# Kernel optimization log

Measured on AMD Instinct MI355X. Metric: run time of the kernel, lower is better.

Reference implementation:

```python
import math
import jax, jax.numpy as jnp
from jax import lax
import numpy as np

TWO_PI = 2.0 * math.pi
CG_ITERS = 30      # DifferentiableLinearSolver(max_iter=30)
CG_TOL = 1e-6
CG_REG = 1e-6      # reg = 1e-6 * I added inside the solver


def build_second_diff_matrix(N, dtype):
    e = jnp.ones(N, dtype)
    e2 = -2.0 * e
    e2 = e2.at[0].set(-1.0).at[-1].set(-1.0)
    oper = jnp.diag(e2) + jnp.diag(e[:-1], -1) + jnp.diag(e[:-1], 1)
    return oper.T @ oper


def cumtrapz(y, dx):
    # cumulative trapezoid along last axis, keeping length (leading zero)
    avg = (y[..., :-1] + y[..., 1:]) * (0.5 * dx)
    c = jnp.cumsum(avg, axis=-1)
    return jnp.concatenate([jnp.zeros_like(y[..., :1]), c], axis=-1)


def differ5(y, delta):
    mid = (y[..., 2:] - y[..., :-2]) / (2.0 * delta)
    first = (y[..., 1:2] - y[..., 0:1]) / delta
    last = (y[..., -1:] - y[..., -2:-1]) / delta
    return jnp.concatenate([first, mid, last], axis=-1)


def projec5(vec, var):
    # per-row norm-ball projection; vec: (B, N)
    M = vec.shape[-1]
    e = jnp.sqrt(M * var)
    n = jnp.linalg.norm(vec, axis=-1, keepdims=True)
    scale = jnp.where(n > e, e / jnp.maximum(n, 1e-30), 1.0)
    return vec * scale


def cg_solve(opedoub, coef, diagv, rhs, x0):
    # Solves (coef*opedoub + diag(diagv) + CG_REG*I) x = rhs via CG,
    # matching torch semantics (early break freezes state).
    def mv(p):
        return coef * (opedoub @ p) + (diagv + CG_REG) * p

    r0 = rhs - mv(x0)
    rs0 = jnp.dot(r0, r0)

    def step(carry, _):
        x, r, p, rsold, done = carry
        Ap = mv(p)
        a = rsold / (jnp.dot(p, Ap) + 1e-12)
        x1 = jnp.where(done, x, x + a * p)
        r1 = jnp.where(done, r, r - a * Ap)
        rsnew = jnp.dot(r1, r1)
        done1 = done | (jnp.sqrt(rsnew) < CG_TOL)
        bta = rsnew / (rsold + 1e-12)
        p1 = jnp.where(done1, p, r1 + bta * p)
        rsold1 = jnp.where(done1, rsold, rsnew)
        return (x1, r1, p1, rsold1, done1), None

    (x, _, _, _, _), _ = lax.scan(step, (x0, r0, r0, rs0, jnp.array(False)), None, length=CG_ITERS)
    return x


def _forward(s, eIF, xm, ym, sum_x, sum_y, lamuda, init_freqs, mode_mask,
             alpha, beta, var, fs, iteration,
             fe_w1, fe_b1, fe_w2, fe_b2,
             pr_w1, pr_b1, pr_w2, pr_b2, pr_w3, pr_b3, iter_weight):
    dtype = s.dtype
    B, N = s.shape
    K = eIF.shape[1]

    # ---- hyperparameter refinement MLP ----
    avg = jnp.mean(init_freqs, axis=1, keepdims=True)              # (B,1)
    h = jax.nn.relu(avg @ fe_w1.T + fe_b1)
    h = jax.nn.relu(h @ fe_w2.T + fe_b2)                            # (B,16)
    cur = jnp.stack([jnp.broadcast_to(alpha, (B,)),
                     jnp.broadcast_to(beta, (B,))], axis=1)         # (B,2)
    z = jnp.concatenate([h, cur], axis=1)                           # (B,18)
    z = jax.nn.relu(z @ pr_w1.T + pr_b1)
    z = jax.nn.relu(z @ pr_w2.T + pr_b2)
    res = jnp.tanh(z @ pr_w3.T + pr_b3)                             # (B,2)
    fac = jax.nn.sigmoid(iter_weight * iteration)
    res = res * fac * 0.1
    new_alpha = jnp.clip(alpha + jnp.mean(res[:, 0] * alpha), 1e-6, 0.01)
    new_beta = jnp.clip(beta + jnp.mean(res[:, 1] * beta), 1e-6, 0.1)

    betathr = jnp.minimum(10.0 ** (iteration / 36.0 - 10.0), new_beta)
    opedoub = build_second_diff_matrix(N, dtype)
    dx = 1.0 / fs

    # Within the torch k-loop, temp sums / lamuda / new_eIF[b,k] all still hold
    # their *input* values, so all (b,k) sub-problems are independent -> vmap.
    u = projec5(s - sum_x - sum_y - lamuda / new_alpha, var)        # (B,N)

    phase = TWO_PI * cumtrapz(eIF, dx)                               # (B,K,N)
    cosm = jnp.cos(phase)
    sinm = jnp.sin(phase)
    resid = (s[:, None, :] - (sum_x[:, None, :] - xm * cosm)
             - (sum_y[:, None, :] - ym * sinm)
             - u[:, None, :] - (lamuda / new_alpha)[:, None, :])
    rhs_x = cosm * resid
    rhs_y = sinm * resid

    coefA = 2.0 / new_alpha
    flat = lambda t: t.reshape(B * K, N)
    cg_v = jax.vmap(cg_solve, in_axes=(None, None, 0, 0, 0))

    xs = cg_v(opedoub, coefA, flat(cosm ** 2), flat(rhs_x), flat(xm)).reshape(B, K, N)
    ys = cg_v(opedoub, coefA, flat(sinm ** 2), flat(rhs_y), flat(ym)).reshape(B, K, N)

    xbar = differ5(xs, dx)
    ybar = differ5(ys, dx)
    denom = xs ** 2 + ys ** 2 + 1e-12
    deltaIF = (xs * ybar - ys * xbar) / (denom * TWO_PI)

    coefS = 2.0 / betathr
    ones_d = jnp.ones((B * K, N), dtype)
    zeros_d = jnp.zeros((B * K, N), dtype)
    smooth = cg_v(opedoub, coefS, ones_d, flat(deltaIF), zeros_d).reshape(B, K, N)
    eIF_s = eIF - 0.5 * smooth

    active = (mode_mask != 0)[:, :, None]                            # (B,K,1)
    new_xm = jnp.where(active, xs, xm)
    new_ym = jnp.where(active, ys, ym)
    new_eIF = jnp.where(active, eIF_s, eIF)

    new_phase = TWO_PI * cumtrapz(new_eIF, dx)
    maskf = active.astype(dtype)
    bsx = jnp.sum(maskf * new_xm * jnp.cos(new_phase), axis=1)       # (B,N)
    bsy = jnp.sum(maskf * new_ym * jnp.sin(new_phase), axis=1)
    new_lamuda = lamuda + new_alpha * (u + bsx + bsy - s)

    return (new_eIF, new_xm, new_ym, bsx, bsy, new_lamuda, new_alpha, new_beta)


def setup_inputs() -> dict:
    key = jax.random.key(0)
    B, K, N = 8, 4, 2048
    ks = jax.random.split(key, 20)
    f32 = jnp.float32
    inp = {
        "s": jax.random.normal(ks[0], (B, N), f32),
        "eIF": 50.0 + 200.0 * jax.random.uniform(ks[1], (B, K, N), f32),
        "xm": 0.1 * jax.random.normal(ks[2], (B, K, N), f32),
        "ym": 0.1 * jax.random.normal(ks[3], (B, K, N), f32),
        "sum_x": 0.1 * jax.random.normal(ks[4], (B, N), f32),
        "sum_y": 0.1 * jax.random.normal(ks[5], (B, N), f32),
        "lamuda": 0.01 * jax.random.normal(ks[6], (B, N), f32),
        "init_freqs": 50.0 + 200.0 * jax.random.uniform(ks[7], (B, K), f32),
        "mode_mask": jnp.ones((B, K), jnp.int32),
        "alpha": jnp.asarray(0.005, f32),
        "beta": jnp.asarray(0.05, f32),
        "var": jnp.asarray(0.01, f32),
        "fs": jnp.asarray(2000.0, f32),
        "iteration": 1,
        # HyperparameterRefinement params (torch Linear: y = x @ W.T + b)
        "fe_w1": 0.1 * jax.random.normal(ks[8], (32, 1), f32),
        "fe_b1": jnp.zeros((32,), f32),
        "fe_w2": 0.1 * jax.random.normal(ks[9], (16, 32), f32),
        "fe_b2": jnp.zeros((16,), f32),
        "pr_w1": 0.1 * jax.random.normal(ks[10], (64, 18), f32),
        "pr_b1": jnp.zeros((64,), f32),
        "pr_w2": 0.1 * jax.random.normal(ks[11], (32, 64), f32),
        "pr_b2": jnp.zeros((32,), f32),
        "pr_w3": 0.1 * jax.random.normal(ks[12], (2, 32), f32),
        "pr_b3": jnp.zeros((2,), f32),
        "iter_weight": jnp.asarray(0.1, f32),
    }
    return inp


def reference(s, eIF, xm, ym, sum_x, sum_y, lamuda, init_freqs, mode_mask,
              alpha, beta, var, fs, iteration,
              fe_w1, fe_b1, fe_w2, fe_b2,
              pr_w1, pr_b1, pr_w2, pr_b2, pr_w3, pr_b3, iter_weight):
    return _forward(s, eIF, xm, ym, sum_x, sum_y, lamuda, init_freqs, mode_mask,
                    alpha, beta, var, fs, iteration,
                    fe_w1, fe_b1, fe_w2, fe_b2,
                    pr_w1, pr_b1, pr_w2, pr_b2, pr_w3, pr_b3, iter_weight)
```

## Files before the change

### kernel.cpp

```cpp
#include <hip/hip_runtime.h>
#include <math.h>

#define Nq 2048
#define Bq 8
#define Kq 4
#define BKq 32
#define NE 16
#define TWO_PI_D 6.283185307179586
#define PI_D 3.141592653589793
#define INV2PI_D 0.15915494309189535


__device__ __forceinline__ double wave_sum_d(double v) {
#pragma unroll
  for (int off = 1; off < 64; off <<= 1) v += __shfl_xor(v, off, 64);
  return v;
}

__device__ __forceinline__ float dpp_sum_f32(float v) {
  v += __int_as_float(__builtin_amdgcn_update_dpp(0, __float_as_int(v), 0x111, 0xf, 0xf, false));
  v += __int_as_float(__builtin_amdgcn_update_dpp(0, __float_as_int(v), 0x112, 0xf, 0xf, false));
  v += __int_as_float(__builtin_amdgcn_update_dpp(0, __float_as_int(v), 0x114, 0xf, 0xe, false));
  v += __int_as_float(__builtin_amdgcn_update_dpp(0, __float_as_int(v), 0x118, 0xf, 0xc, false));
  v += __int_as_float(__builtin_amdgcn_update_dpp(0, __float_as_int(v), 0x142, 0xa, 0xf, false));
  v += __int_as_float(__builtin_amdgcn_update_dpp(0, __float_as_int(v), 0x143, 0xc, 0xf, false));
  return __int_as_float(__builtin_amdgcn_readlane(__float_as_int(v), 63));
}

__device__ __forceinline__ float dpp_up1(float v) {
  return __int_as_float(__builtin_amdgcn_update_dpp(0, __float_as_int(v), 0x138, 0xf, 0xf, false));
}
__device__ __forceinline__ float dpp_dn1(float v) {
  return __int_as_float(__builtin_amdgcn_update_dpp(0, __float_as_int(v), 0x130, 0xf, 0xf, false));
}

__device__ __forceinline__ double lane_excl_prefix_d(double T, int lane) {
  double acc = T;
#pragma unroll
  for (int off = 1; off < 64; off <<= 1) {
    double t = __shfl_up(acc, off, 64);
    if (lane >= off) acc += t;
  }
  return acc - T;
}

__device__ __forceinline__ void fast_sincos_ph(double ph, float* sn, float* cs) {
  double k = trunc(ph * INV2PI_D);
  float phr = (float)(ph - k * TWO_PI_D);
  __sincosf(phr, sn, cs);
}

template <bool UNIT>
__device__ __forceinline__ void applyA16(const float* p, float* Ap,
                                         const float* dd, float c, float c3,
                                         float c4, float ddu, float hL0,
                                         float hL1, float hR0, float hR1,
                                         int lane, int half) {
  float lm1 = dpp_up1(p[NE - 1]);
  float lm2 = dpp_up1(p[NE - 2]);
  float rp1 = dpp_dn1(p[0]);
  float rp2 = dpp_dn1(p[1]);
  if (lane == 0) { lm1 = hL1; lm2 = hL0; }
  if (lane == 63) { rp1 = hR0; rp2 = hR1; }
#pragma unroll
  for (int e = 0; e < NE; ++e) {
    float m2 = (e >= 2) ? p[e - 2] : (e == 1 ? lm1 : lm2);
    float m1 = (e >= 1) ? p[e - 1] : lm1;
    float q1 = (e <= NE - 2) ? p[e + 1] : rp1;
    float q2 = (e <= NE - 3) ? p[e + 2] : (e == NE - 2 ? rp1 : rp2);
    float u = fmaf(c, m2 + q2, -(c4 * (m1 + q1)));
    Ap[e] = fmaf(UNIT ? ddu : dd[e], p[e], u);
  }
  if (half == 0 && lane == 0) {
    float d0 = (UNIT ? ddu : dd[0]) - c4;
    Ap[0] = fmaf(d0, p[0], fmaf(c, p[2], -(c3 * p[1])));
    float d1 = UNIT ? ddu : dd[1];
    Ap[1] = fmaf(d1, p[1], -(c3 * p[0])) + fmaf(c, p[3], -(c4 * p[2]));
  }
  if (half == 1 && lane == 63) {
    float dm2 = UNIT ? ddu : dd[NE - 2];
    Ap[NE - 2] = fmaf(dm2, p[NE - 2], c * p[NE - 4]) -
                 fmaf(c4, p[NE - 3], c3 * p[NE - 1]);
    float dm1 = (UNIT ? ddu : dd[NE - 1]) - c4;
    Ap[NE - 1] = fmaf(dm1, p[NE - 1], c * p[NE - 3]) - c3 * p[NE - 2];
  }
}

template <bool UNIT>
__device__ __forceinline__ void cg_wave2(float coef, float* dd, float* r,
                                         float* x, float hxL0, float hxL1,
                                         float hxR0, float hxR1, int lane,
                                         int half, int wv,
                                         float (*sh_part)[4],
                                         float (*sh_rb)[2]) {
  const float c = coef, c3 = 3.0f * coef, c4 = 4.0f * coef;
  const float ddu = 6.0f * coef + (1.0f + 1e-6f);
  if (!UNIT) {
#pragma unroll
    for (int e = 0; e < NE; ++e) dd[e] += 6.0f * coef;
  }
  const int nb = wv ^ 1;
  float p[NE], Ap[NE];
  applyA16<UNIT>(x, Ap, dd, c, c3, c4, ddu, hxL0, hxL1, hxR0, hxR1, lane, half);
  float s0 = 0.f, s1 = 0.f;
#pragma unroll
  for (int e = 0; e < NE; ++e) {
    r[e] -= Ap[e];
    p[e] = r[e];
    ((e & 1) ? s1 : s0) = fmaf(r[e], r[e], (e & 1) ? s1 : s0);
  }
  float rsp = dpp_sum_f32(s0 + s1);
  if (lane == 0) sh_part[wv][3] = rsp;
  if (half == 0) {
    if (lane == 63) { sh_rb[wv][0] = r[NE - 2]; sh_rb[wv][1] = r[NE - 1]; }
  } else {
    if (lane == 0) { sh_rb[wv][0] = r[0]; sh_rb[wv][1] = r[1]; }
  }
  __syncthreads();
  float rs = rsp + sh_part[nb][3];
  float hL0 = 0.f, hL1 = 0.f, hR0 = 0.f, hR1 = 0.f;
  if (half == 1) { hL0 = sh_rb[nb][0]; hL1 = sh_rb[nb][1]; }
  else { hR0 = sh_rb[nb][0]; hR1 = sh_rb[nb][1]; }
  bool done = false;
  for (int it = 0; it < 30; ++it) {
    applyA16<UNIT>(p, Ap, dd, c, c3, c4, ddu, hL0, hL1, hR0, hR1, lane, half);
    float pa0 = 0.f, pa1 = 0.f, aa0 = 0.f, aa1 = 0.f, ra0 = 0.f, ra1 = 0.f;
#pragma unroll
    for (int e = 0; e < NE; ++e) {
      if (e & 1) {
        pa1 = fmaf(p[e], Ap[e], pa1);
        aa1 = fmaf(Ap[e], Ap[e], aa1);
        ra1 = fmaf(r[e], Ap[e], ra1);
      } else {
        pa0 = fmaf(p[e], Ap[e], pa0);
        aa0 = fmaf(Ap[e], Ap[e], aa0);
        ra0 = fmaf(r[e], Ap[e], ra0);
      }
    }
    float papp = dpp_sum_f32(pa0 + pa1);
    float aapp = dpp_sum_f32(aa0 + aa1);
    float rapp = dpp_sum_f32(ra0 + ra1);
    if (lane == 0) {
      sh_part[wv][0] = papp;
      sh_part[wv][1] = aapp;
      sh_part[wv][2] = rapp;
    }
    __syncthreads();
    float pap = papp + sh_part[nb][0];
    float apap = aapp + sh_part[nb][1];
    float rap = rapp + sh_part[nb][2];
    float a = __fdividef(rs, pap + 1e-12f);
    float rsnew = fmaf(a * a, apap, fmaf(-2.0f * a, rap, rs));
    if (!done) {
#pragma unroll
      for (int e = 0; e < NE; ++e) {
        x[e] = fmaf(a, p[e], x[e]);
        r[e] = fmaf(-a, Ap[e], r[e]);
      }
    }
    bool done1 = done || (rsnew < 1e-12f);
    float bta = __fdividef(rsnew, rs + 1e-12f);
    if (!done1) {
#pragma unroll
      for (int e = 0; e < NE; ++e) p[e] = fmaf(bta, p[e], r[e]);
      rs = rsnew;
      if (half == 0) {
        if (lane == 63) { sh_rb[wv][0] = r[NE - 2]; sh_rb[wv][1] = r[NE - 1]; }
      } else {
        if (lane == 0) { sh_rb[wv][0] = r[0]; sh_rb[wv][1] = r[1]; }
      }
    }
    __syncthreads();
    if (!done1) {
      if (half == 1) {
        hL0 = fmaf(bta, hL0, sh_rb[nb][0]);
        hL1 = fmaf(bta, hL1, sh_rb[nb][1]);
      } else {
        hR0 = fmaf(bta, hR0, sh_rb[nb][0]);
        hR1 = fmaf(bta, hR1, sh_rb[nb][1]);
      }
    }
    done = done1;
  }
}

__device__ __forceinline__ double blk_reduce(double v, double* sh) {
#pragma unroll
  for (int off = 32; off > 0; off >>= 1) v += __shfl_down(v, off, 64);
  int wid = threadIdx.x >> 6;
  int lane = threadIdx.x & 63;
  __syncthreads();
  if (lane == 0) sh[wid] = v;
  __syncthreads();
  double r = sh[0] + sh[1] + sh[2] + sh[3];
  __syncthreads();
  return r;
}

__global__ __launch_bounds__(256, 1) void row_kernel(
    const float* __restrict__ s, const float* __restrict__ eIF,
    const float* __restrict__ xm, const float* __restrict__ ym,
    const float* __restrict__ sum_x, const float* __restrict__ sum_y,
    const float* __restrict__ lamuda, const float* __restrict__ init_freqs,
    const int* __restrict__ mode_mask, const float* __restrict__ alpha_p,
    const float* __restrict__ beta_p, const float* __restrict__ var_p,
    const float* __restrict__ fs_p, const int* __restrict__ iter_p,
    const float* __restrict__ fe_w1, const float* __restrict__ fe_b1,
    const float* __restrict__ fe_w2, const float* __restrict__ fe_b2,
    const float* __restrict__ pr_w1, const float* __restrict__ pr_b1,
    const float* __restrict__ pr_w2, const float* __restrict__ pr_b2,
    const float* __restrict__ pr_w3, const float* __restrict__ pr_b3,
    const float* __restrict__ iter_w_p, double* __restrict__ hdr,
    float* __restrict__ out_eIF, float* __restrict__ out_xm,
    float* __restrict__ out_ym, float* __restrict__ cx_w,
    float* __restrict__ cy_w, float* __restrict__ out_scal) {
  __shared__ double sh_avg[Bq];
  __shared__ double sh_h1[Bq][32];
  __shared__ double sh_z[Bq][18];
  __shared__ double sh_z1[Bq][64];
  __shared__ double sh_z2[Bq][32];
  __shared__ double sh_res[Bq][2];
  __shared__ double sh_hdr[4];
  __shared__ double sh_sc[8];
  __shared__ float sh_part[4][4];
  __shared__ float sh_rb[4][2];
  __shared__ float sh_xs[Nq], sh_ys[Nq];

  const int tid = threadIdx.x;
  const int wv = tid >> 6, lane = tid & 63;
  const int pair = wv >> 1, half = wv & 1;
  const int row = blockIdx.x, b = row >> 2;
  const int bb = b * Nq, base = row * Nq;
  const int seg0 = half * 1024;

  double alpha = (double)alpha_p[0], beta = (double)beta_p[0];
  double iterv = (double)iter_p[0];
  if (tid < Bq) {
    double avg = 0.0;
#pragma unroll
    for (int k = 0; k < Kq; ++k) avg += (double)init_freqs[tid * Kq + k];
    sh_avg[tid] = avg * (1.0 / Kq);
  }
  __syncthreads();
  {
    int b2 = tid >> 5, j = tid & 31;
    double v = (double)fe_w1[j] * sh_avg[b2] + (double)fe_b1[j];
    sh_h1[b2][j] = v > 0.0 ? v : 0.0;
  }
  __syncthreads();
  if (tid < 128) {
    int b2 = tid >> 4, j = tid & 15;
    double acc = (double)fe_b2[j];
    for (int i = 0; i < 32; ++i) acc += (double)fe_w2[j * 32 + i] * sh_h1[b2][i];
    sh_z[b2][j] = acc > 0.0 ? acc : 0.0;
  }
  if (tid >= 128 && tid < 128 + Bq) {
    sh_z[tid - 128][16] = alpha;
    sh_z[tid - 128][17] = beta;
  }
  __syncthreads();
  for (int n = tid; n < 512; n += 256) {
    int b2 = n >> 6, j = n & 63;
    double acc = (double)pr_b1[j];
    for (int i = 0; i < 18; ++i) acc += (double)pr_w1[j * 18 + i] * sh_z[b2][i];
    sh_z1[b2][j] = acc > 0.0 ? acc : 0.0;
  }
  __syncthreads();
  {
    int b2 = tid >> 5, j = tid & 31;
    double acc = (double)pr_b2[j];
    for (int i = 0; i < 64; ++i) acc += (double)pr_w2[j * 64 + i] * sh_z1[b2][i];
    sh_z2[b2][j] = acc > 0.0 ? acc : 0.0;
  }
  __syncthreads();
  if (tid < 16) {
    int b2 = tid >> 1, c = tid & 1;
    double acc = (double)pr_b3[c];
    for (int i = 0; i < 32; ++i) acc += (double)pr_w3[c * 32 + i] * sh_z2[b2][i];
    double fac = 1.0 / (1.0 + exp(-(double)iter_w_p[0] * iterv));
    sh_res[b2][c] = tanh(acc) * fac * 0.1;
  }
  __syncthreads();
  if (tid == 0) {
    double r0 = 0.0, r1 = 0.0;
    for (int q = 0; q < Bq; ++q) { r0 += sh_res[q][0]; r1 += sh_res[q][1]; }
    double na = fmin(fmax(alpha + r0 * alpha * (1.0 / Bq), 1e-6), 0.01);
    double nb2 = fmin(fmax(beta + r1 * beta * (1.0 / Bq), 1e-6), 0.1);
    double betathr = fmin(pow(10.0, iterv / 36.0 - 10.0), nb2);
    sh_hdr[0] = na;
    sh_hdr[1] = 2.0 / na;
    sh_hdr[2] = 2.0 / betathr;
    sh_hdr[3] = 1.0 / na;
    hdr[0] = na;
    hdr[4] = 1.0 / na;
    out_scal[0] = (float)na;
    out_scal[1] = (float)nb2;
  }
  __syncthreads();
  const float coefA = (float)sh_hdr[1];
  const float coefS = (float)sh_hdr[2];
  const double inva = sh_hdr[3];

  double tv[NE];
  {
    double n0 = 0.0;
#pragma unroll
    for (int e = 0; e < NE; ++e) {
      int gi = bb + seg0 + lane * NE + e;
      tv[e] = (double)s[gi] - (double)sum_x[gi] - (double)sum_y[gi] -
              (double)lamuda[gi] * inva;
      n0 += tv[e] * tv[e];
    }
    double np = wave_sum_d(n0);
    if (pair == 0 && lane == 0) sh_sc[4 + half] = np;
  }
  const double dx = 1.0 / (double)fs_p[0];
  const double c0 = PI_D * dx;
  double ev[NE], pl[NE];
#pragma unroll
  for (int e = 0; e < NE; ++e) ev[e] = (double)eIF[base + seg0 + lane * NE + e];
  pl[0] = ev[0];
#pragma unroll
  for (int e = 1; e < NE; ++e) pl[e] = pl[e - 1] + ev[e];
  double offs_w = lane_excl_prefix_d(pl[NE - 1], lane);
  {
    double segT = __shfl(offs_w + pl[NE - 1], 63, 64);
    if (pair == 0 && lane == 0) sh_sc[half] = segT;
    if (pair == 0 && half == 0 && lane == 0) sh_sc[2] = ev[0];
  }
  __syncthreads();
  double offs = offs_w + (half ? sh_sc[0] : 0.0);
  double y0 = sh_sc[2];
  {
    double nsq = sh_sc[4] + sh_sc[5];
    double nn = sqrt(nsq);
    double ee = sqrt((double)Nq * (double)var_p[0]);
    double scale = (nn > ee) ? ee / fmax(nn, 1e-30) : 1.0;
    double oms = 1.0 - scale;
#pragma unroll
    for (int e = 0; e < NE; ++e) tv[e] *= oms;
  }

  float dd[NE], r[NE], x[NE];
#pragma unroll
  for (int e = 0; e < NE; ++e) {
    int i = seg0 + lane * NE + e;
    double ph = c0 * (2.0 * (offs + pl[e]) - ev[e] - y0);
    float sn, cs;
    fast_sincos_ph(ph, &sn, &cs);
    float xmv = xm[base + i], ymv = ym[base + i];
    double resid = tv[e] + (double)xmv * (double)cs + (double)ymv * (double)sn;
    if (pair == 0) {
      dd[e] = cs * cs + 1e-6f;
      r[e] = (float)((double)cs * resid);
      x[e] = xmv;
    } else {
      dd[e] = sn * sn + 1e-6f;
      r[e] = (float)((double)sn * resid);
      x[e] = ymv;
    }
  }
  {
    const float* src = (pair == 0) ? (xm + base) : (ym + base);
    float hxL0 = 0.f, hxL1 = 0.f, hxR0 = 0.f, hxR1 = 0.f;
    if (half == 0) { hxR0 = src[1024]; hxR1 = src[1025]; }
    else { hxL0 = src[1022]; hxL1 = src[1023]; }
    cg_wave2<false>(coefA, dd, r, x, hxL0, hxL1, hxR0, hxR1, lane, half, wv,
                    sh_part, sh_rb);
  }

  {
    float* dst = (pair == 0) ? sh_xs : sh_ys;
#pragma unroll
    for (int e = 0; e < NE; ++e) dst[seg0 + lane * NE + e] = x[e];
  }
  __syncthreads();

  {
    float invdx = (float)fs_p[0], inv2dx = 0.5f * invdx;
#pragma unroll
    for (int e = 0; e < NE; ++e) {
      int i = seg0 + lane * NE + e;
      float xc = sh_xs[i], yc = sh_ys[i];
      float xb, yb;
      if (i == 0) {
        xb = (sh_xs[1] - sh_xs[0]) * invdx;
        yb = (sh_ys[1] - sh_ys[0]) * invdx;
      } else if (i == Nq - 1) {
        xb = (sh_xs[Nq - 1] - sh_xs[Nq - 2]) * invdx;
        yb = (sh_ys[Nq - 1] - sh_ys[Nq - 2]) * invdx;
      } else {
        xb = (sh_xs[i + 1] - sh_xs[i - 1]) * inv2dx;
        yb = (sh_ys[i + 1] - sh_ys[i - 1]) * inv2dx;
      }
      float denom = xc * xc + yc * yc + 1e-12f;
      r[e] = (xc * yb - yc * xb) / (denom * (float)TWO_PI_D);
      x[e] = 0.0f;
    }
  }
  __syncthreads();

  cg_wave2<true>(coefS, nullptr, r, x, 0.f, 0.f, 0.f, 0.f, lane, half, wv,
                 sh_part, sh_rb);

  bool active = mode_mask[row] != 0;
  double eifn[NE];
#pragma unroll
  for (int e = 0; e < NE; ++e) {
    int i = seg0 + lane * NE + e;
    double eifv = (double)eIF[base + i];
    eifn[e] = active ? (eifv - 0.5 * (double)x[e]) : eifv;
  }
  if (pair == 0) {
#pragma unroll
    for (int e = 0; e < NE; ++e) {
      int i = seg0 + lane * NE + e;
      out_eIF[base + i] = (float)eifn[e];
      out_xm[base + i] = active ? sh_xs[i] : xm[base + i];
    }
  } else {
#pragma unroll
    for (int e = 0; e < NE; ++e) {
      int i = seg0 + lane * NE + e;
      out_ym[base + i] = active ? sh_ys[i] : ym[base + i];
    }
  }
  pl[0] = eifn[0];
#pragma unroll
  for (int e = 1; e < NE; ++e) pl[e] = pl[e - 1] + eifn[e];
  offs_w = lane_excl_prefix_d(pl[NE - 1], lane);
  {
    double segT = __shfl(offs_w + pl[NE - 1], 63, 64);
    if (pair == 0 && half == 0 && lane == 0) sh_sc[6] = segT;
    if (pair == 0 && half == 0 && lane == 0) sh_sc[3] = eifn[0];
  }
  __syncthreads();
  {
    double offs2 = offs_w + (half ? sh_sc[6] : 0.0);
    double y02 = sh_sc[3];
#pragma unroll
    for (int e = 0; e < NE; ++e) {
      int i = seg0 + lane * NE + e;
      double ph = c0 * (2.0 * (offs2 + pl[e]) - eifn[e] - y02);
      float sn, cs;
      fast_sincos_ph(ph, &sn, &cs);
      if (pair == 0)
        cx_w[base + i] = active ? sh_xs[i] * cs : 0.0f;
      else
        cy_w[base + i] = active ? sh_ys[i] * sn : 0.0f;
    }
  }
}

__global__ __launch_bounds__(256) void final_kernel(
    const float* __restrict__ s, const float* __restrict__ sum_x,
    const float* __restrict__ sum_y, const float* __restrict__ lamuda,
    const float* __restrict__ var_p, const double* __restrict__ hdr,
    const float* __restrict__ cx_w, const float* __restrict__ cy_w,
    float* __restrict__ out_bsx, float* __restrict__ out_bsy,
    float* __restrict__ out_lam) {
  __shared__ double sh_red[4];
  __shared__ double sh_scale;
  int b = blockIdx.x;
  int bb = b * Nq;
  int tid = threadIdx.x;
  double na = hdr[0], inva = hdr[4];
  double t[8];
  double loc = 0.0;
#pragma unroll
  for (int e = 0; e < 8; ++e) {
    int gi = bb + tid + e * 256;
    t[e] = (double)s[gi] - (double)sum_x[gi] - (double)sum_y[gi] -
           (double)lamuda[gi] * inva;
    loc += t[e] * t[e];
  }
  double nsq = blk_reduce(loc, sh_red);
  if (tid == 0) {
    double n = sqrt(nsq);
    double ee = sqrt((double)Nq * (double)var_p[0]);
    sh_scale = (n > ee) ? ee / fmax(n, 1e-30) : 1.0;
  }
  __syncthreads();
  double scale = sh_scale;
#pragma unroll
  for (int e = 0; e < 8; ++e) {
    int i = tid + e * 256;
    int gi = bb + i;
    double bx = 0.0, by = 0.0;
#pragma unroll
    for (int k = 0; k < Kq; ++k) {
      bx += (double)cx_w[(b * Kq + k) * Nq + i];
      by += (double)cy_w[(b * Kq + k) * Nq + i];
    }
    double u = t[e] * scale;
    double nl = (double)lamuda[gi] + na * (u + bx + by - (double)s[gi]);
    out_bsx[gi] = (float)bx;
    out_bsy[gi] = (float)by;
    out_lam[gi] = (float)nl;
  }
}

extern "C" void kernel_launch(void* const* d_in, const int* in_sizes, int n_in,
                              void* d_out, int out_size, void* d_ws, size_t ws_size,
                              hipStream_t stream) {
  (void)in_sizes; (void)n_in; (void)out_size; (void)ws_size;
  const float* s = (const float*)d_in[0];
  const float* eIF = (const float*)d_in[1];
  const float* xm = (const float*)d_in[2];
  const float* ym = (const float*)d_in[3];
  const float* sum_x = (const float*)d_in[4];
  const float* sum_y = (const float*)d_in[5];
  const float* lamuda = (const float*)d_in[6];
  const float* init_freqs = (const float*)d_in[7];
  const int* mode_mask = (const int*)d_in[8];
  const float* alpha = (const float*)d_in[9];
  const float* beta = (const float*)d_in[10];
  const float* var = (const float*)d_in[11];
  const float* fs = (const float*)d_in[12];
  const int* iteration = (const int*)d_in[13];
  const float* fe_w1 = (const float*)d_in[14];
  const float* fe_b1 = (const float*)d_in[15];
  const float* fe_w2 = (const float*)d_in[16];
  const float* fe_b2 = (const float*)d_in[17];
  const float* pr_w1 = (const float*)d_in[18];
  const float* pr_b1 = (const float*)d_in[19];
  const float* pr_w2 = (const float*)d_in[20];
  const float* pr_b2 = (const float*)d_in[21];
  const float* pr_w3 = (const float*)d_in[22];
  const float* pr_b3 = (const float*)d_in[23];
  const float* iter_weight = (const float*)d_in[24];

  float* out = (float*)d_out;
  const int BN = Bq * Nq;
  const int BKN = BKq * Nq;
  float* out_eIF = out;
  float* out_xm = out + BKN;
  float* out_ym = out + 2 * BKN;
  float* out_bsx = out + 3 * BKN;
  float* out_bsy = out + 3 * BKN + BN;
  float* out_lam = out + 3 * BKN + 2 * BN;
  float* out_scal = out + 3 * BKN + 3 * BN;

  double* W = (double*)d_ws;
  double* hdr = W;
  float* F = (float*)(W + 16);
  float* cx_w = F;
  float* cy_w = F + BKN;

  row_kernel<<<BKq, 256, 0, stream>>>(
      s, eIF, xm, ym, sum_x, sum_y, lamuda, init_freqs, mode_mask, alpha, beta,
      var, fs, iteration, fe_w1, fe_b1, fe_w2, fe_b2, pr_w1, pr_b1, pr_w2,
      pr_b2, pr_w3, pr_b3, iter_weight, hdr, out_eIF, out_xm, out_ym, cx_w,
      cy_w, out_scal);
  final_kernel<<<Bq, 256, 0, stream>>>(s, sum_x, sum_y, lamuda, var, hdr, cx_w,
                                       cy_w, out_bsx, out_bsy, out_lam);
}
```

Before: 173.7 us.

## Fuse row and final kernels into one per-batch 1024-thread mega kernel

Replaces the two-kernel design (32 row blocks of 256 threads plus a final reduction kernel) with a single kernel of 8 blocks of 1024 threads. Each block covers one batch and its 4 modes, with 4 waves per row and 8 elements per lane. The x and y CG solves are interleaved in one loop, and halo exchange uses double-buffered shared memory with one barrier per iteration instead of two. The mode sum goes through shared-memory atomics rather than a global workspace, which removes the second launch and the global round-trip. The cost is fewer blocks (8 vs 32) on a large GPU and block-wide barriers across 16 waves.

Result: slower. 324.8 us (+87.0%).

```diff
diff --git a/kernel.cpp b/kernel.cpp
--- a/kernel.cpp
+++ b/kernel.cpp
@@ -4,8 +4,8 @@
 #define Nq 2048
 #define Bq 8
 #define Kq 4
-#define BKq 32
-#define NE 16
+#define NE 8
+#define SEG 512
 #define TWO_PI_D 6.283185307179586
 #define PI_D 3.141592653589793
 #define INV2PI_D 0.15915494309189535
@@ -51,16 +51,16 @@
 }
 
 template <bool UNIT>
-__device__ __forceinline__ void applyA16(const float* p, float* Ap,
-                                         const float* dd, float c, float c3,
-                                         float c4, float ddu, float hL0,
-                                         float hL1, float hR0, float hR1,
-                                         int lane, int half) {
+__device__ __forceinline__ void applyA8(const float* p, float* Ap,
+                                        const float* dd, float ddu, float c,
+                                        float c3, float c4, float hL0, float hL1,
+                                        float hR0, float hR1, int lane,
+                                        bool isF, bool isL) {
   float lm1 = dpp_up1(p[NE - 1]);
   float lm2 = dpp_up1(p[NE - 2]);
   float rp1 = dpp_dn1(p[0]);
   float rp2 = dpp_dn1(p[1]);
-  if (lane == 0) { lm1 = hL1; lm2 = hL0; }
+  if (lane == 0) { lm2 = hL0; lm1 = hL1; }
   if (lane == 63) { rp1 = hR0; rp2 = hR1; }
 #pragma unroll
   for (int e = 0; e < NE; ++e) {
@@ -71,13 +71,13 @@
     float u = fmaf(c, m2 + q2, -(c4 * (m1 + q1)));
     Ap[e] = fmaf(UNIT ? ddu : dd[e], p[e], u);
   }
-  if (half == 0 && lane == 0) {
+  if (isF && lane == 0) {
     float d0 = (UNIT ? ddu : dd[0]) - c4;
     Ap[0] = fmaf(d0, p[0], fmaf(c, p[2], -(c3 * p[1])));
     float d1 = UNIT ? ddu : dd[1];
     Ap[1] = fmaf(d1, p[1], -(c3 * p[0])) + fmaf(c, p[3], -(c4 * p[2]));
   }
-  if (half == 1 && lane == 63) {
+  if (isL && lane == 63) {
     float dm2 = UNIT ? ddu : dd[NE - 2];
     Ap[NE - 2] = fmaf(dm2, p[NE - 2], c * p[NE - 4]) -
                  fmaf(c4, p[NE - 3], c3 * p[NE - 1]);
@@ -86,71 +86,220 @@
   }
 }
 
-template <bool UNIT>
-__device__ __forceinline__ void cg_wave2(float coef, float* dd, float* r,
-                                         float* x, float hxL0, float hxL1,
-                                         float hxR0, float hxR1, int lane,
-                                         int half, int wv,
-                                         float (*sh_part)[4],
-                                         float (*sh_rb)[2]) {
-  const float c = coef, c3 = 3.0f * coef, c4 = 4.0f * coef;
-  const float ddu = 6.0f * coef + (1.0f + 1e-6f);
-  if (!UNIT) {
-#pragma unroll
-    for (int e = 0; e < NE; ++e) dd[e] += 6.0f * coef;
-  }
-  const int nb = wv ^ 1;
+__device__ void cg_dual(float coef, float* ddX, float* rX, float* xX,
+                        float* ddY, float* rY, float* xY, const float* hx,
+                        int lane, int lw, int rr, float* P, float* E) {
+  const float c = coef, c3 = 3.f * coef, c4 = 4.f * coef;
+  const bool isF = (lw == 0), isL = (lw == 3);
+#pragma unroll
+  for (int e = 0; e < NE; ++e) {
+    ddX[e] += 6.f * coef;
+    ddY[e] += 6.f * coef;
+  }
+  float pX[NE], ApX[NE], pY[NE], ApY[NE];
+  applyA8<false>(xX, ApX, ddX, 0.f, c, c3, c4, hx[0], hx[1], hx[4], hx[5], lane, isF, isL);
+  applyA8<false>(xY, ApY, ddY, 0.f, c, c3, c4, hx[2], hx[3], hx[6], hx[7], lane, isF, isL);
+  float sX = 0.f, sY = 0.f;
+#pragma unroll
+  for (int e = 0; e < NE; ++e) {
+    rX[e] -= ApX[e]; pX[e] = rX[e]; sX = fmaf(rX[e], rX[e], sX);
+    rY[e] -= ApY[e]; pY[e] = rY[e]; sY = fmaf(rY[e], rY[e], sY);
+  }
+  sX = dpp_sum_f32(sX);
+  sY = dpp_sum_f32(sY);
+  {
+    float* pt = P + (rr * 4 + lw) * 8;
+    float* ed = E + (rr * 4 + lw) * 8;
+    if (lane == 0) {
+      pt[0] = sX; pt[1] = sY;
+      ed[0] = rX[0]; ed[1] = rX[1]; ed[2] = rY[0]; ed[3] = rY[1];
+    }
+    if (lane == 63) {
+      ed[4] = rX[NE - 2]; ed[5] = rX[NE - 1]; ed[6] = rY[NE - 2]; ed[7] = rY[NE - 1];
+    }
+  }
+  __syncthreads();
+  float rsX = 0.f, rsY = 0.f;
+#pragma unroll
+  for (int w = 0; w < 4; ++w) {
+    const float* q = P + (rr * 4 + w) * 8;
+    rsX += q[0]; rsY += q[1];
+  }
+  float hrLX0 = 0, hrLX1 = 0, hpLX0 = 0, hpLX1 = 0;
+  float hrLY0 = 0, hrLY1 = 0, hpLY0 = 0, hpLY1 = 0;
+  float hrRX0 = 0, hrRX1 = 0, hpRX0 = 0, hpRX1 = 0;
+  float hrRY0 = 0, hrRY1 = 0, hpRY0 = 0, hpRY1 = 0;
+  if (!isF) {
+    const float* ed = E + (rr * 4 + lw - 1) * 8;
+    hrLX0 = ed[4]; hrLX1 = ed[5]; hrLY0 = ed[6]; hrLY1 = ed[7];
+    hpLX0 = hrLX0; hpLX1 = hrLX1; hpLY0 = hrLY0; hpLY1 = hrLY1;
+  }
+  if (!isL) {
+    const float* ed = E + (rr * 4 + lw + 1) * 8;
+    hrRX0 = ed[0]; hrRX1 = ed[1]; hrRY0 = ed[2]; hrRY1 = ed[3];
+    hpRX0 = hrRX0; hpRX1 = hrRX1; hpRY0 = hrRY0; hpRY1 = hrRY1;
+  }
+  bool dX = false, dY = false;
+  for (int t = 0; t < 30; ++t) {
+    int par = (t + 1) & 1;
+    float* Pb = P + par * 128;
+    float* Eb = E + par * 128;
+    applyA8<false>(pX, ApX, ddX, 0.f, c, c3, c4, hpLX0, hpLX1, hpRX0, hpRX1, lane, isF, isL);
+    applyA8<false>(pY, ApY, ddY, 0.f, c, c3, c4, hpLY0, hpLY1, hpRY0, hpRY1, lane, isF, isL);
+    float paX = 0, aaX = 0, raX = 0, paY = 0, aaY = 0, raY = 0;
+#pragma unroll
+    for (int e = 0; e < NE; ++e) {
+      paX = fmaf(pX[e], ApX[e], paX);
+      aaX = fmaf(ApX[e], ApX[e], aaX);
+      raX = fmaf(rX[e], ApX[e], raX);
+      paY = fmaf(pY[e], ApY[e], paY);
+      aaY = fmaf(ApY[e], ApY[e], aaY);
+      raY = fmaf(rY[e], ApY[e], raY);
+    }
+    paX = dpp_sum_f32(paX); aaX = dpp_sum_f32(aaX); raX = dpp_sum_f32(raX);
+    paY = dpp_sum_f32(paY); aaY = dpp_sum_f32(aaY); raY = dpp_sum_f32(raY);
+    {
+      float* pt = Pb + (rr * 4 + lw) * 8;
+      float* ed = Eb + (rr * 4 + lw) * 8;
+      if (lane == 0) {
+        pt[0] = paX; pt[1] = aaX; pt[2] = raX; pt[3] = paY; pt[4] = aaY; pt[5] = raY;
+        ed[0] = ApX[0]; ed[1] = ApX[1]; ed[2] = ApY[0]; ed[3] = ApY[1];
+      }
+      if (lane == 63) {
+        ed[4] = ApX[NE - 2]; ed[5] = ApX[NE - 1]; ed[6] = ApY[NE - 2]; ed[7] = ApY[NE - 1];
+      }
+    }
+    __syncthreads();
+    float PpX = 0, AaX = 0, RaX = 0, PpY = 0, AaY = 0, RaY = 0;
+#pragma unroll
+    for (int w = 0; w < 4; ++w) {
+      const float* q = Pb + (rr * 4 + w) * 8;
+      PpX += q[0]; AaX += q[1]; RaX += q[2];
+      PpY += q[3]; AaY += q[4]; RaY += q[5];
+    }
+    float aX = __fdividef(rsX, PpX + 1e-12f);
+    float rsnX = fmaf(aX * aX, AaX, fmaf(-2.f * aX, RaX, rsX));
+    float aY = __fdividef(rsY, PpY + 1e-12f);
+    float rsnY = fmaf(aY * aY, AaY, fmaf(-2.f * aY, RaY, rsY));
+    if (!dX) {
+#pragma unroll
+      for (int e = 0; e < NE; ++e) {
+        xX[e] = fmaf(aX, pX[e], xX[e]);
+        rX[e] = fmaf(-aX, ApX[e], rX[e]);
+      }
+    }
+    if (!dY) {
+#pragma unroll
+      for (int e = 0; e < NE; ++e) {
+        xY[e] = fmaf(aY, pY[e], xY[e]);
+        rY[e] = fmaf(-aY, ApY[e], rY[e]);
+      }
+    }
+    bool d1X = dX || (rsnX < 1e-12f);
+    bool d1Y = dY || (rsnY < 1e-12f);
+    float btaX = __fdividef(rsnX, rsX + 1e-12f);
+    float btaY = __fdividef(rsnY, rsY + 1e-12f);
+    if (!d1X) {
+#pragma unroll
+      for (int e = 0; e < NE; ++e) pX[e] = fmaf(btaX, pX[e], rX[e]);
+      rsX = rsnX;
+      if (!isF) {
+        const float* eL = Eb + (rr * 4 + lw - 1) * 8;
+        hrLX0 = fmaf(-aX, eL[4], hrLX0); hpLX0 = fmaf(btaX, hpLX0, hrLX0);
+        hrLX1 = fmaf(-aX, eL[5], hrLX1); hpLX1 = fmaf(btaX, hpLX1, hrLX1);
+      }
+      if (!isL) {
+        const float* eR = Eb + (rr * 4 + lw + 1) * 8;
+        hrRX0 = fmaf(-aX, eR[0], hrRX0); hpRX0 = fmaf(btaX, hpRX0, hrRX0);
+        hrRX1 = fmaf(-aX, eR[1], hrRX1); hpRX1 = fmaf(btaX, hpRX1, hrRX1);
+      }
+    }
+    if (!d1Y) {
+#pragma unroll
+      for (int e = 0; e < NE; ++e) pY[e] = fmaf(btaY, pY[e], rY[e]);
+      rsY = rsnY;
+      if (!isF) {
+        const float* eL = Eb + (rr * 4 + lw - 1) * 8;
+        hrLY0 = fmaf(-aY, eL[6], hrLY0); hpLY0 = fmaf(btaY, hpLY0, hrLY0);
+        hrLY1 = fmaf(-aY, eL[7], hrLY1); hpLY1 = fmaf(btaY, hpLY1, hrLY1);
+      }
+      if (!isL) {
+        const float* eR = Eb + (rr * 4 + lw + 1) * 8;
+        hrRY0 = fmaf(-aY, eR[2], hrRY0); hpRY0 = fmaf(btaY, hpRY0, hrRY0);
+        hrRY1 = fmaf(-aY, eR[3], hrRY1); hpRY1 = fmaf(btaY, hpRY1, hrRY1);
+      }
+    }
+    dX = d1X;
+    dY = d1Y;
+  }
+}
+
+__device__ void cg_single(float coef, float* r, float* x, int lane, int lw,
+                          int rr, float* P, float* E) {
+  const float c = coef, c3 = 3.f * coef, c4 = 4.f * coef;
+  const float ddu = 6.f * coef + (1.0f + 1e-6f);
+  const bool isF = (lw == 0), isL = (lw == 3);
   float p[NE], Ap[NE];
-  applyA16<UNIT>(x, Ap, dd, c, c3, c4, ddu, hxL0, hxL1, hxR0, hxR1, lane, half);
-  float s0 = 0.f, s1 = 0.f;
+  applyA8<true>(x, Ap, nullptr, ddu, c, c3, c4, 0.f, 0.f, 0.f, 0.f, lane, isF, isL);
+  float s0 = 0.f;
 #pragma unroll
   for (int e = 0; e < NE; ++e) {
     r[e] -= Ap[e];
     p[e] = r[e];
-    ((e & 1) ? s1 : s0) = fmaf(r[e], r[e], (e & 1) ? s1 : s0);
-  }
-  float rsp = dpp_sum_f32(s0 + s1);
-  if (lane == 0) sh_part[wv][3] = rsp;
-  if (half == 0) {
-    if (lane == 63) { sh_rb[wv][0] = r[NE - 2]; sh_rb[wv][1] = r[NE - 1]; }
-  } else {
-    if (lane == 0) { sh_rb[wv][0] = r[0]; sh_rb[wv][1] = r[1]; }
-  }
-  __syncthreads();
-  float rs = rsp + sh_part[nb][3];
-  float hL0 = 0.f, hL1 = 0.f, hR0 = 0.f, hR1 = 0.f;
-  if (half == 1) { hL0 = sh_rb[nb][0]; hL1 = sh_rb[nb][1]; }
-  else { hR0 = sh_rb[nb][0]; hR1 = sh_rb[nb][1]; }
+    s0 = fmaf(r[e], r[e], s0);
+  }
+  s0 = dpp_sum_f32(s0);
+  {
+    float* pt = P + (rr * 4 + lw) * 8;
+    float* ed = E + (rr * 4 + lw) * 8;
+    if (lane == 0) { pt[0] = s0; ed[0] = r[0]; ed[1] = r[1]; }
+    if (lane == 63) { ed[4] = r[NE - 2]; ed[5] = r[NE - 1]; }
+  }
+  __syncthreads();
+  float rs = 0.f;
+#pragma unroll
+  for (int w = 0; w < 4; ++w) rs += (P + (rr * 4 + w) * 8)[0];
+  float hrL0 = 0, hrL1 = 0, hpL0 = 0, hpL1 = 0;
+  float hrR0 = 0, hrR1 = 0, hpR0 = 0, hpR1 = 0;
+  if (!isF) {
+    const float* ed = E + (rr * 4 + lw - 1) * 8;
+    hrL0 = ed[4]; hrL1 = ed[5]; hpL0 = hrL0; hpL1 = hrL1;
+  }
+  if (!isL) {
+    const float* ed = E + (rr * 4 + lw + 1) * 8;
+    hrR0 = ed[0]; hrR1 = ed[1]; hpR0 = hrR0; hpR1 = hrR1;
+  }
   bool done = false;
-  for (int it = 0; it < 30; ++it) {
-    applyA16<UNIT>(p, Ap, dd, c, c3, c4, ddu, hL0, hL1, hR0, hR1, lane, half);
-    float pa0 = 0.f, pa1 = 0.f, aa0 = 0.f, aa1 = 0.f, ra0 = 0.f, ra1 = 0.f;
+  for (int t = 0; t < 30; ++t) {
+    int par = (t + 1) & 1;
+    float* Pb = P + par * 128;
+    float* Eb = E + par * 128;
+    applyA8<true>(p, Ap, nullptr, ddu, c, c3, c4, hpL0, hpL1, hpR0, hpR1, lane, isF, isL);
+    float pa = 0, aa = 0, ra = 0;
 #pragma unroll
     for (int e = 0; e < NE; ++e) {
-      if (e & 1) {
-        pa1 = fmaf(p[e], Ap[e], pa1);
-        aa1 = fmaf(Ap[e], Ap[e], aa1);
-        ra1 = fmaf(r[e], Ap[e], ra1);
-      } else {
-        pa0 = fmaf(p[e], Ap[e], pa0);
-        aa0 = fmaf(Ap[e], Ap[e], aa0);
-        ra0 = fmaf(r[e], Ap[e], ra0);
-      }
-    }
-    float papp = dpp_sum_f32(pa0 + pa1);
-    float aapp = dpp_sum_f32(aa0 + aa1);
-    float rapp = dpp_sum_f32(ra0 + ra1);
-    if (lane == 0) {
-      sh_part[wv][0] = papp;
-      sh_part[wv][1] = aapp;
-      sh_part[wv][2] = rapp;
+      pa = fmaf(p[e], Ap[e], pa);
+      aa = fmaf(Ap[e], Ap[e], aa);
+      ra = fmaf(r[e], Ap[e], ra);
+    }
+    pa = dpp_sum_f32(pa);
+    aa = dpp_sum_f32(aa);
+    ra = dpp_sum_f32(ra);
+    {
+      float* pt = Pb + (rr * 4 + lw) * 8;
+      float* ed = Eb + (rr * 4 + lw) * 8;
+      if (lane == 0) { pt[0] = pa; pt[1] = aa; pt[2] = ra; ed[0] = Ap[0]; ed[1] = Ap[1]; }
+      if (lane == 63) { ed[4] = Ap[NE - 2]; ed[5] = Ap[NE - 1]; }
     }
     __syncthreads();
-    float pap = papp + sh_part[nb][0];
-    float apap = aapp + sh_part[nb][1];
-    float rap = rapp + sh_part[nb][2];
-    float a = __fdividef(rs, pap + 1e-12f);
-    float rsnew = fmaf(a * a, apap, fmaf(-2.0f * a, rap, rs));
+    float Pp = 0, Aa = 0, Ra = 0;
+#pragma unroll
+    for (int w = 0; w < 4; ++w) {
+      const float* q = Pb + (rr * 4 + w) * 8;
+      Pp += q[0]; Aa += q[1]; Ra += q[2];
+    }
+    float a = __fdividef(rs, Pp + 1e-12f);
+    float rsn = fmaf(a * a, Aa, fmaf(-2.f * a, Ra, rs));
     if (!done) {
 #pragma unroll
       for (int e = 0; e < NE; ++e) {
@@ -158,46 +307,28 @@
         r[e] = fmaf(-a, Ap[e], r[e]);
       }
     }
-    bool done1 = done || (rsnew < 1e-12f);
-    float bta = __fdividef(rsnew, rs + 1e-12f);
-    if (!done1) {
+    bool d1 = done || (rsn < 1e-12f);
+    float bta = __fdividef(rsn, rs + 1e-12f);
+    if (!d1) {
 #pragma unroll
       for (int e = 0; e < NE; ++e) p[e] = fmaf(bta, p[e], r[e]);
-      rs = rsnew;
-      if (half == 0) {
-        if (lane == 63) { sh_rb[wv][0] = r[NE - 2]; sh_rb[wv][1] = r[NE - 1]; }
-      } else {
-        if (lane == 0) { sh_rb[wv][0] = r[0]; sh_rb[wv][1] = r[1]; }
-      }
-    }
-    __syncthreads();
-    if (!done1) {
-      if (half == 1) {
-        hL0 = fmaf(bta, hL0, sh_rb[nb][0]);
-        hL1 = fmaf(bta, hL1, sh_rb[nb][1]);
-      } else {
-        hR0 = fmaf(bta, hR0, sh_rb[nb][0]);
-        hR1 = fmaf(bta, hR1, sh_rb[nb][1]);
-      }
-    }
-    done = done1;
-  }
-}
-
-__device__ __forceinline__ double blk_reduce(double v, double* sh) {
-#pragma unroll
-  for (int off = 32; off > 0; off >>= 1) v += __shfl_down(v, off, 64);
-  int wid = threadIdx.x >> 6;
-  int lane = threadIdx.x & 63;
-  __syncthreads();
-  if (lane == 0) sh[wid] = v;
-  __syncthreads();
-  double r = sh[0] + sh[1] + sh[2] + sh[3];
-  __syncthreads();
-  return r;
-}
-
-__global__ __launch_bounds__(256, 1) void row_kernel(
+      rs = rsn;
+      if (!isF) {
+        const float* eL = Eb + (rr * 4 + lw - 1) * 8;
+        hrL0 = fmaf(-a, eL[4], hrL0); hpL0 = fmaf(bta, hpL0, hrL0);
+        hrL1 = fmaf(-a, eL[5], hrL1); hpL1 = fmaf(bta, hpL1, hrL1);
+      }
+      if (!isL) {
+        const float* eR = Eb + (rr * 4 + lw + 1) * 8;
+        hrR0 = fmaf(-a, eR[0], hrR0); hpR0 = fmaf(bta, hpR0, hrR0);
+        hrR1 = fmaf(-a, eR[1], hrR1); hpR1 = fmaf(bta, hpR1, hrR1);
+      }
+    }
+    done = d1;
+  }
+}
+
+__global__ __launch_bounds__(1024) void mega_kernel(
     const float* __restrict__ s, const float* __restrict__ eIF,
     const float* __restrict__ xm, const float* __restrict__ ym,
     const float* __restrict__ sum_x, const float* __restrict__ sum_y,
@@ -210,28 +341,38 @@
     const float* __restrict__ pr_w1, const float* __restrict__ pr_b1,
     const float* __restrict__ pr_w2, const float* __restrict__ pr_b2,
     const float* __restrict__ pr_w3, const float* __restrict__ pr_b3,
-    const float* __restrict__ iter_w_p, double* __restrict__ hdr,
-    float* __restrict__ out_eIF, float* __restrict__ out_xm,
-    float* __restrict__ out_ym, float* __restrict__ cx_w,
-    float* __restrict__ cy_w, float* __restrict__ out_scal) {
+    const float* __restrict__ iter_w_p, float* __restrict__ out_eIF,
+    float* __restrict__ out_xm, float* __restrict__ out_ym,
+    float* __restrict__ out_bsx, float* __restrict__ out_bsy,
+    float* __restrict__ out_lam, float* __restrict__ out_scal) {
   __shared__ double sh_avg[Bq];
   __shared__ double sh_h1[Bq][32];
-  __shared__ double sh_z[Bq][18];
+  __shared__ double sh_zz[Bq][18];
   __shared__ double sh_z1[Bq][64];
   __shared__ double sh_z2[Bq][32];
   __shared__ double sh_res[Bq][2];
   __shared__ double sh_hdr[4];
-  __shared__ double sh_sc[8];
-  __shared__ float sh_part[4][4];
-  __shared__ float sh_rb[4][2];
-  __shared__ float sh_xs[Nq], sh_ys[Nq];
+  __shared__ double sh_un[4];
+  __shared__ double sh_segT[4][4], sh_y0v[4];
+  __shared__ double sh_segT2[4][4], sh_y02v[4];
+  __shared__ float sh_part[2 * 128];
+  __shared__ float sh_edge[2 * 128];
+  __shared__ float sh_exy[4 * 4 * 4];
+  __shared__ float sh_bsx[Nq], sh_bsy[Nq];
 
   const int tid = threadIdx.x;
   const int wv = tid >> 6, lane = tid & 63;
-  const int pair = wv >> 1, half = wv & 1;
-  const int row = blockIdx.x, b = row >> 2;
+  const int rr = wv >> 2, lw = wv & 3;
+  const int b = blockIdx.x;
+  const int row = b * Kq + rr;
   const int bb = b * Nq, base = row * Nq;
-  const int seg0 = half * 1024;
+  const int seg0 = lw * SEG;
+  const bool isF = (lw == 0), isL = (lw == 3);
+
+  for (int j = tid; j < Nq; j += 1024) {
+    sh_bsx[j] = 0.f;
+    sh_bsy[j] = 0.f;
+  }
 
   double alpha = (double)alpha_p[0], beta = (double)beta_p[0];
   double iterv = (double)iter_p[0];
@@ -242,7 +383,7 @@
     sh_avg[tid] = avg * (1.0 / Kq);
   }
   __syncthreads();
-  {
+  if (tid < 256) {
     int b2 = tid >> 5, j = tid & 31;
     double v = (double)fe_w1[j] * sh_avg[b2] + (double)fe_b1[j];
     sh_h1[b2][j] = v > 0.0 ? v : 0.0;
@@ -252,21 +393,21 @@
     int b2 = tid >> 4, j = tid & 15;
     double acc = (double)fe_b2[j];
     for (int i = 0; i < 32; ++i) acc += (double)fe_w2[j * 32 + i] * sh_h1[b2][i];
-    sh_z[b2][j] = acc > 0.0 ? acc : 0.0;
+    sh_zz[b2][j] = acc > 0.0 ? acc : 0.0;
   }
   if (tid >= 128 && tid < 128 + Bq) {
-    sh_z[tid - 128][16] = alpha;
-    sh_z[tid - 128][17] = beta;
-  }
-  __syncthreads();
-  for (int n = tid; n < 512; n += 256) {
-    int b2 = n >> 6, j = n & 63;
+    sh_zz[tid - 128][16] = alpha;
+    sh_zz[tid - 128][17] = beta;
+  }
+  __syncthreads();
+  if (tid < 512) {
+    int b2 = tid >> 6, j = tid & 63;
     double acc = (double)pr_b1[j];
-    for (int i = 0; i < 18; ++i) acc += (double)pr_w1[j * 18 + i] * sh_z[b2][i];
+    for (int i = 0; i < 18; ++i) acc += (double)pr_w1[j * 18 + i] * sh_zz[b2][i];
     sh_z1[b2][j] = acc > 0.0 ? acc : 0.0;
   }
   __syncthreads();
-  {
+  if (tid < 256) {
     int b2 = tid >> 5, j = tid & 31;
     double acc = (double)pr_b2[j];
     for (int i = 0; i < 64; ++i) acc += (double)pr_w2[j * 64 + i] * sh_z1[b2][i];
@@ -283,7 +424,10 @@
   __syncthreads();
   if (tid == 0) {
     double r0 = 0.0, r1 = 0.0;
-    for (int q = 0; q < Bq; ++q) { r0 += sh_res[q][0]; r1 += sh_res[q][1]; }
+    for (int q = 0; q < Bq; ++q) {
+      r0 += sh_res[q][0];
+      r1 += sh_res[q][1];
+    }
     double na = fmin(fmax(alpha + r0 * alpha * (1.0 / Bq), 1e-6), 0.01);
     double nb2 = fmin(fmax(beta + r1 * beta * (1.0 / Bq), 1e-6), 0.1);
     double betathr = fmin(pow(10.0, iterv / 36.0 - 10.0), nb2);
@@ -291,10 +435,10 @@
     sh_hdr[1] = 2.0 / na;
     sh_hdr[2] = 2.0 / betathr;
     sh_hdr[3] = 1.0 / na;
-    hdr[0] = na;
-    hdr[4] = 1.0 / na;
-    out_scal[0] = (float)na;
-    out_scal[1] = (float)nb2;
+    if (blockIdx.x == 0) {
+      out_scal[0] = (float)na;
+      out_scal[1] = (float)nb2;
+    }
   }
   __syncthreads();
   const float coefA = (float)sh_hdr[1];
@@ -312,7 +456,7 @@
       n0 += tv[e] * tv[e];
     }
     double np = wave_sum_d(n0);
-    if (pair == 0 && lane == 0) sh_sc[4 + half] = np;
+    if (rr == 0 && lane == 0) sh_un[lw] = np;
   }
   const double dx = 1.0 / (double)fs_p[0];
   const double c0 = PI_D * dx;
@@ -325,14 +469,16 @@
   double offs_w = lane_excl_prefix_d(pl[NE - 1], lane);
   {
     double segT = __shfl(offs_w + pl[NE - 1], 63, 64);
-    if (pair == 0 && lane == 0) sh_sc[half] = segT;
-    if (pair == 0 && half == 0 && lane == 0) sh_sc[2] = ev[0];
-  }
-  __syncthreads();
-  double offs = offs_w + (half ? sh_sc[0] : 0.0);
-  double y0 = sh_sc[2];
-  {
-    double nsq = sh_sc[4] + sh_sc[5];
+    if (lane == 0) sh_segT[rr][lw] = segT;
+    if (isF && lane == 0) sh_y0v[rr] = ev[0];
+  }
+  __syncthreads();
+  double offs = offs_w;
+  for (int w = 0; w < 3; ++w)
+    if (lw > w) offs += sh_segT[rr][w];
+  double y0 = sh_y0v[rr];
+  {
+    double nsq = sh_un[0] + sh_un[1] + sh_un[2] + sh_un[3];
     double nn = sqrt(nsq);
     double ee = sqrt((double)Nq * (double)var_p[0]);
     double scale = (nn > ee) ? ee / fmax(nn, 1e-30) : 1.0;
@@ -341,7 +487,7 @@
     for (int e = 0; e < NE; ++e) tv[e] *= oms;
   }
 
-  float dd[NE], r[NE], x[NE];
+  float ddX[NE], rX[NE], xX[NE], ddY[NE], rY[NE], xY[NE];
 #pragma unroll
   for (int e = 0; e < NE; ++e) {
     int i = seg0 + lane * NE + e;
@@ -350,58 +496,74 @@
     fast_sincos_ph(ph, &sn, &cs);
     float xmv = xm[base + i], ymv = ym[base + i];
     double resid = tv[e] + (double)xmv * (double)cs + (double)ymv * (double)sn;
-    if (pair == 0) {
-      dd[e] = cs * cs + 1e-6f;
-      r[e] = (float)((double)cs * resid);
-      x[e] = xmv;
-    } else {
-      dd[e] = sn * sn + 1e-6f;
-      r[e] = (float)((double)sn * resid);
-      x[e] = ymv;
-    }
-  }
-  {
-    const float* src = (pair == 0) ? (xm + base) : (ym + base);
-    float hxL0 = 0.f, hxL1 = 0.f, hxR0 = 0.f, hxR1 = 0.f;
-    if (half == 0) { hxR0 = src[1024]; hxR1 = src[1025]; }
-    else { hxL0 = src[1022]; hxL1 = src[1023]; }
-    cg_wave2<false>(coefA, dd, r, x, hxL0, hxL1, hxR0, hxR1, lane, half, wv,
-                    sh_part, sh_rb);
-  }
-
-  {
-    float* dst = (pair == 0) ? sh_xs : sh_ys;
-#pragma unroll
-    for (int e = 0; e < NE; ++e) dst[seg0 + lane * NE + e] = x[e];
-  }
-  __syncthreads();
-
+    ddX[e] = cs * cs + 1e-6f;
+    rX[e] = (float)((double)cs * resid);
+    xX[e] = xmv;
+    ddY[e] = sn * sn + 1e-6f;
+    rY[e] = (float)((double)sn * resid);
+    xY[e] = ymv;
+  }
+  float hx[8] = {0, 0, 0, 0, 0, 0, 0, 0};
+  if (!isF) {
+    hx[0] = xm[base + seg0 - 2];
+    hx[1] = xm[base + seg0 - 1];
+    hx[2] = ym[base + seg0 - 2];
+    hx[3] = ym[base + seg0 - 1];
+  }
+  if (!isL) {
+    hx[4] = xm[base + seg0 + SEG];
+    hx[5] = xm[base + seg0 + SEG + 1];
+    hx[6] = ym[base + seg0 + SEG];
+    hx[7] = ym[base + seg0 + SEG + 1];
+  }
+
+  cg_dual(coefA, ddX, rX, xX, ddY, rY, xY, hx, lane, lw, rr, sh_part, sh_edge);
+
+  {
+    float* ex = sh_exy + (rr * 4 + lw) * 4;
+    if (lane == 0) { ex[0] = xX[0]; ex[1] = xY[0]; }
+    if (lane == 63) { ex[2] = xX[NE - 1]; ex[3] = xY[NE - 1]; }
+  }
+  __syncthreads();
   {
     float invdx = (float)fs_p[0], inv2dx = 0.5f * invdx;
+    float xl = dpp_up1(xX[NE - 1]), xr = dpp_dn1(xX[0]);
+    float yl = dpp_up1(xY[NE - 1]), yr = dpp_dn1(xY[0]);
+    if (!isF && lane == 0) {
+      const float* ex = sh_exy + (rr * 4 + lw - 1) * 4;
+      xl = ex[2];
+      yl = ex[3];
+    }
+    if (!isL && lane == 63) {
+      const float* ex = sh_exy + (rr * 4 + lw + 1) * 4;
+      xr = ex[0];
+      yr = ex[1];
+    }
 #pragma unroll
     for (int e = 0; e < NE; ++e) {
       int i = seg0 + lane * NE + e;
-      float xc = sh_xs[i], yc = sh_ys[i];
+      float xm1 = (e >= 1) ? xX[e - 1] : xl;
+      float xp1 = (e <= NE - 2) ? xX[e + 1] : xr;
+      float ym1 = (e >= 1) ? xY[e - 1] : yl;
+      float yp1 = (e <= NE - 2) ? xY[e + 1] : yr;
       float xb, yb;
       if (i == 0) {
-        xb = (sh_xs[1] - sh_xs[0]) * invdx;
-        yb = (sh_ys[1] - sh_ys[0]) * invdx;
+        xb = (xp1 - xX[e]) * invdx;
+        yb = (yp1 - xY[e]) * invdx;
       } else if (i == Nq - 1) {
-        xb = (sh_xs[Nq - 1] - sh_xs[Nq - 2]) * invdx;
-        yb = (sh_ys[Nq - 1] - sh_ys[Nq - 2]) * invdx;
+        xb = (xX[e] - xm1) * invdx;
+        yb = (xY[e] - ym1) * invdx;
       } else {
-        xb = (sh_xs[i + 1] - sh_xs[i - 1]) * inv2dx;
-        yb = (sh_ys[i + 1] - sh_ys[i - 1]) * inv2dx;
-      }
-      float denom = xc * xc + yc * yc + 1e-12f;
-      r[e] = (xc * yb - yc * xb) / (denom * (float)TWO_PI_D);
-      x[e] = 0.0f;
-    }
-  }
-  __syncthreads();
-
-  cg_wave2<true>(coefS, nullptr, r, x, 0.f, 0.f, 0.f, 0.f, lane, half, wv,
-                 sh_part, sh_rb);
+        xb = (xp1 - xm1) * inv2dx;
+        yb = (yp1 - ym1) * inv2dx;
+      }
+      float denom = xX[e] * xX[e] + xY[e] * xY[e] + 1e-12f;
+      rX[e] = (xX[e] * yb - xY[e] * xb) / (denom * (float)TWO_PI_D);
+      ddX[e] = 0.0f;
+    }
+  }
+
+  cg_single(coefS, rX, ddX, lane, lw, rr, sh_part, sh_edge);
 
   bool active = mode_mask[row] != 0;
   double eifn[NE];
@@ -409,21 +571,10 @@
   for (int e = 0; e < NE; ++e) {
     int i = seg0 + lane * NE + e;
     double eifv = (double)eIF[base + i];
-    eifn[e] = active ? (eifv - 0.5 * (double)x[e]) : eifv;
-  }
-  if (pair == 0) {
-#pragma unroll
-    for (int e = 0; e < NE; ++e) {
-      int i = seg0 + lane * NE + e;
-      out_eIF[base + i] = (float)eifn[e];
-      out_xm[base + i] = active ? sh_xs[i] : xm[base + i];
-    }
-  } else {
-#pragma unroll
-    for (int e = 0; e < NE; ++e) {
-      int i = seg0 + lane * NE + e;
-      out_ym[base + i] = active ? sh_ys[i] : ym[base + i];
-    }
+    eifn[e] = active ? (eifv - 0.5 * (double)ddX[e]) : eifv;
+    out_eIF[base + i] = (float)eifn[e];
+    out_xm[base + i] = active ? xX[e] : xm[base + i];
+    out_ym[base + i] = active ? xY[e] : ym[base + i];
   }
   pl[0] = eifn[0];
 #pragma unroll
@@ -431,79 +582,55 @@
   offs_w = lane_excl_prefix_d(pl[NE - 1], lane);
   {
     double segT = __shfl(offs_w + pl[NE - 1], 63, 64);
-    if (pair == 0 && half == 0 && lane == 0) sh_sc[6] = segT;
-    if (pair == 0 && half == 0 && lane == 0) sh_sc[3] = eifn[0];
-  }
-  __syncthreads();
-  {
-    double offs2 = offs_w + (half ? sh_sc[6] : 0.0);
-    double y02 = sh_sc[3];
+    if (lane == 0) sh_segT2[rr][lw] = segT;
+    if (isF && lane == 0) sh_y02v[rr] = eifn[0];
+  }
+  __syncthreads();
+  {
+    double offs2 = offs_w;
+    for (int w = 0; w < 3; ++w)
+      if (lw > w) offs2 += sh_segT2[rr][w];
+    double y02 = sh_y02v[rr];
 #pragma unroll
     for (int e = 0; e < NE; ++e) {
       int i = seg0 + lane * NE + e;
       double ph = c0 * (2.0 * (offs2 + pl[e]) - eifn[e] - y02);
       float sn, cs;
       fast_sincos_ph(ph, &sn, &cs);
-      if (pair == 0)
-        cx_w[base + i] = active ? sh_xs[i] * cs : 0.0f;
-      else
-        cy_w[base + i] = active ? sh_ys[i] * sn : 0.0f;
-    }
-  }
-}
-
-__global__ __launch_bounds__(256) void final_kernel(
-    const float* __restrict__ s, const float* __restrict__ sum_x,
-    const float* __restrict__ sum_y, const float* __restrict__ lamuda,
-    const float* __restrict__ var_p, const double* __restrict__ hdr,
-    const float* __restrict__ cx_w, const float* __restrict__ cy_w,
-    float* __restrict__ out_bsx, float* __restrict__ out_bsy,
-    float* __restrict__ out_lam) {
-  __shared__ double sh_red[4];
-  __shared__ double sh_scale;
-  int b = blockIdx.x;
-  int bb = b * Nq;
-  int tid = threadIdx.x;
-  double na = hdr[0], inva = hdr[4];
-  double t[8];
-  double loc = 0.0;
-#pragma unroll
-  for (int e = 0; e < 8; ++e) {
-    int gi = bb + tid + e * 256;
-    t[e] = (double)s[gi] - (double)sum_x[gi] - (double)sum_y[gi] -
-           (double)lamuda[gi] * inva;
-    loc += t[e] * t[e];
-  }
-  double nsq = blk_reduce(loc, sh_red);
-  if (tid == 0) {
-    double n = sqrt(nsq);
+      if (active) {
+        atomicAdd(&sh_bsx[i], xX[e] * cs);
+        atomicAdd(&sh_bsy[i], xY[e] * sn);
+      }
+    }
+  }
+  __syncthreads();
+
+  {
+    double na = sh_hdr[0];
+    double nsq = sh_un[0] + sh_un[1] + sh_un[2] + sh_un[3];
+    double nn = sqrt(nsq);
     double ee = sqrt((double)Nq * (double)var_p[0]);
-    sh_scale = (n > ee) ? ee / fmax(n, 1e-30) : 1.0;
-  }
-  __syncthreads();
-  double scale = sh_scale;
-#pragma unroll
-  for (int e = 0; e < 8; ++e) {
-    int i = tid + e * 256;
-    int gi = bb + i;
-    double bx = 0.0, by = 0.0;
-#pragma unroll
-    for (int k = 0; k < Kq; ++k) {
-      bx += (double)cx_w[(b * Kq + k) * Nq + i];
-      by += (double)cy_w[(b * Kq + k) * Nq + i];
-    }
-    double u = t[e] * scale;
-    double nl = (double)lamuda[gi] + na * (u + bx + by - (double)s[gi]);
-    out_bsx[gi] = (float)bx;
-    out_bsy[gi] = (float)by;
-    out_lam[gi] = (float)nl;
+    double scale = (nn > ee) ? ee / fmax(nn, 1e-30) : 1.0;
+#pragma unroll
+    for (int j = 0; j < 2; ++j) {
+      int i = tid + j * 1024;
+      int gi = bb + i;
+      double t = (double)s[gi] - (double)sum_x[gi] - (double)sum_y[gi] -
+                 (double)lamuda[gi] * inva;
+      double u = t * scale;
+      double bx = (double)sh_bsx[i], by = (double)sh_bsy[i];
+      double nl = (double)lamuda[gi] + na * (u + bx + by - (double)s[gi]);
+      out_bsx[gi] = (float)bx;
+      out_bsy[gi] = (float)by;
+      out_lam[gi] = (float)nl;
+    }
   }
 }
 
 extern "C" void kernel_launch(void* const* d_in, const int* in_sizes, int n_in,
                               void* d_out, int out_size, void* d_ws, size_t ws_size,
                               hipStream_t stream) {
-  (void)in_sizes; (void)n_in; (void)out_size; (void)ws_size;
+  (void)in_sizes; (void)n_in; (void)out_size; (void)d_ws; (void)ws_size;
   const float* s = (const float*)d_in[0];
   const float* eIF = (const float*)d_in[1];
   const float* xm = (const float*)d_in[2];
@@ -532,7 +659,7 @@
 
   float* out = (float*)d_out;
   const int BN = Bq * Nq;
-  const int BKN = BKq * Nq;
+  const int BKN = 4 * BN;
   float* out_eIF = out;
   float* out_xm = out + BKN;
   float* out_ym = out + 2 * BKN;
@@ -541,17 +668,9 @@
   float* out_lam = out + 3 * BKN + 2 * BN;
   float* out_scal = out + 3 * BKN + 3 * BN;
 
-  double* W = (double*)d_ws;
-  double* hdr = W;
-  float* F = (float*)(W + 16);
-  float* cx_w = F;
-  float* cy_w = F + BKN;
-
-  row_kernel<<<BKq, 256, 0, stream>>>(
+  mega_kernel<<<Bq, 1024, 0, stream>>>(
       s, eIF, xm, ym, sum_x, sum_y, lamuda, init_freqs, mode_mask, alpha, beta,
       var, fs, iteration, fe_w1, fe_b1, fe_w2, fe_b2, pr_w1, pr_b1, pr_w2,
-      pr_b2, pr_w3, pr_b3, iter_weight, hdr, out_eIF, out_xm, out_ym, cx_w,
-      cy_w, out_scal);
-  final_kernel<<<Bq, 256, 0, stream>>>(s, sum_x, sum_y, lamuda, var, hdr, cx_w,
-                                       cy_w, out_bsx, out_bsy, out_lam);
-}
+      pr_b2, pr_w3, pr_b3, iter_weight, out_eIF, out_xm, out_ym, out_bsx,
+      out_bsy, out_lam, out_scal);
+}
```
